# Optimization experiments

Hardware: AMD Instinct MI355X
Metric: run time of the kernel (lower is better)

Reference implementation:

```python
import jax, jax.numpy as jnp
import numpy as np

N = 50000   # nodes
E = 800000  # edges (avg degree 16)
D = 128     # feature dim
H = 4       # heads
DH = D // H # head dim


def setup_inputs() -> dict:
    key = jax.random.key(0)
    ks = jax.random.split(key, 12)
    s = 1.0 / np.sqrt(D)
    return {
        "x": jax.random.normal(ks[0], (N, D), dtype=jnp.float32),
        "src": jax.random.randint(ks[1], (E,), 0, N, dtype=jnp.int32),
        "dst": jax.random.randint(ks[2], (E,), 0, N, dtype=jnp.int32),
        # input_linear: Linear(d, d)
        "W_in": jax.random.uniform(ks[3], (D, D), jnp.float32, -s, s),
        "b_in": jax.random.uniform(ks[4], (D,), jnp.float32, -s, s),
        # attn_linear_u: Linear(d, n_heads), attn_linear_v: Linear(d, n_heads, bias=False)
        "W_au": jax.random.uniform(ks[5], (D, H), jnp.float32, -s, s),
        "b_au": jax.random.uniform(ks[6], (H,), jnp.float32, -s, s),
        "W_av": jax.random.uniform(ks[7], (D, H), jnp.float32, -s, s),
        # FFN: Linear(d, d) -> ReLU -> Linear(d, d)  (dropout=0)
        "W_f1": jax.random.uniform(ks[8], (D, D), jnp.float32, -s, s),
        "b_f1": jax.random.uniform(ks[9], (D,), jnp.float32, -s, s),
        "W_f2": jax.random.uniform(ks[10], (D, D), jnp.float32, -s, s),
        "b_f2": jax.random.uniform(ks[11], (D,), jnp.float32, -s, s),
    }


def reference(x, src, dst, W_in, b_in, W_au, b_au, W_av, W_f1, b_f1, W_f2, b_f2):
    h = x @ W_in + b_in                                # [N, D]
    su = h @ W_au + b_au                               # [N, H]
    sv = h @ W_av                                      # [N, H]
    # u_add_v gather + LeakyReLU
    e = jax.nn.leaky_relu(su[src] + sv[dst], 0.2)      # [E, H]
    # edge_softmax: softmax over incoming edges of each dst node
    m = jax.ops.segment_max(e, dst, num_segments=N)    # [N, H]
    ex = jnp.exp(e - m[dst])                           # [E, H]
    z = jax.ops.segment_sum(ex, dst, num_segments=N)   # [N, H]
    p = ex / z[dst]                                    # [E, H]
    # u_mul_e_sum: weighted aggregation (note reshape order (N, d_head, H))
    hu = h.reshape(N, DH, H)[src]                      # [E, DH, H]
    agg = jax.ops.segment_sum(hu * p[:, None, :], dst, num_segments=N)  # [N, DH, H]
    y = agg.reshape(N, D)
    # FFN
    return jax.nn.relu(y @ W_f1 + b_f1) @ W_f2 + b_f2
```

## Files before the change

### kernel.cpp

```cpp
#include <hip/hip_runtime.h>
#include <hip/hip_bf16.h>
#include <math.h>

#define D 128
#define NHEADS 4

static constexpr int CAP  = 64;
static constexpr int CAPB = 5120;
static constexpr int EB   = 4096;

typedef __attribute__((ext_vector_type(8))) short bf16x8;
typedef __attribute__((ext_vector_type(4))) float f32x4;

__device__ __forceinline__ float4 ld4(const float* p) {
    return *reinterpret_cast<const float4*>(p);
}
__device__ __forceinline__ float4 fma4(float a, float4 b, float4 c) {
    c.x = fmaf(a, b.x, c.x); c.y = fmaf(a, b.y, c.y);
    c.z = fmaf(a, b.z, c.z); c.w = fmaf(a, b.w, c.w);
    return c;
}
__device__ __forceinline__ unsigned short f2bf(float f) {
    __hip_bfloat16 b = __float2bfloat16(f);
    return __builtin_bit_cast(unsigned short, b);
}
__device__ __forceinline__ float bf2f(unsigned short u) {
    return __uint_as_float((unsigned)u << 16);
}
__device__ __forceinline__ void cvt_hilo(const float4& a0, const float4& a1,
                                         bf16x8& hi, bf16x8& lo) {
    float v[8] = {a0.x, a0.y, a0.z, a0.w, a1.x, a1.y, a1.z, a1.w};
#pragma unroll
    for (int i = 0; i < 8; ++i) {
        unsigned short h = f2bf(v[i]);
        hi[i] = (short)h;
        lo[i] = (short)f2bf(v[i] - bf2f(h));
    }
}

__global__ __launch_bounds__(256)
void clear_kernel(int* __restrict__ bucket_cnt, int nb16) {
    for (int i = threadIdx.x; i < nb16; i += 256) bucket_cnt[i] = 0;
}

template<int MODE>
__global__ __launch_bounds__(256)
void mfma_gemm128(const float* __restrict__ A, const float* __restrict__ W,
                  const float* __restrict__ bias, float* __restrict__ out,
                  unsigned short* __restrict__ out16, int N, int ntiles)
{
    __shared__ unsigned short wh[D * D];
    __shared__ unsigned short wl[D * D];

    const int t = threadIdx.x;
#pragma unroll
    for (int i = 0; i < 16; ++i) {
        int g = t + i * 256;
        int col = g & 127;
        int k0 = (g >> 7) << 2;
        short4 h4, l4;
#pragma unroll
        for (int k = 0; k < 4; ++k) {
            float v = W[(size_t)(k0 + k) * D + col];
            unsigned short hb = f2bf(v);
            ((short*)&h4)[k] = (short)hb;
            ((short*)&l4)[k] = (short)f2bf(v - bf2f(hb));
        }
        int off = col * D + (k0 ^ ((col & 7) << 3));
        *reinterpret_cast<short4*>(&wh[off]) = h4;
        *reinterpret_cast<short4*>(&wl[off]) = l4;
    }
    __syncthreads();

    const int wid  = t >> 6;
    const int lane = t & 63;
    const int q8   = (lane >> 4) * 8;

    for (int tile = blockIdx.x; tile < ntiles; tile += gridDim.x) {
        const int rbase = tile * 64 + wid * 16;
        const int arow  = rbase + (lane & 15);

        bf16x8 ahi[4], alo[4];
#pragma unroll
        for (int ks = 0; ks < 4; ++ks) {
            float4 a0 = {0, 0, 0, 0}, a1 = {0, 0, 0, 0};
            if (arow < N) {
                const float* ap = A + (size_t)arow * D + 32 * ks + q8;
                a0 = ld4(ap); a1 = ld4(ap + 4);
            }
            cvt_hilo(a0, a1, ahi[ks], alo[ks]);
        }

        f32x4 acc[8];
#pragma unroll
        for (int ct = 0; ct < 8; ++ct) acc[ct] = (f32x4){0.f, 0.f, 0.f, 0.f};

#pragma unroll
        for (int ct = 0; ct < 8; ++ct) {
            const int colb = ct * 16 + (lane & 15);
            const int sw   = (colb & 7) << 3;
            bf16x8 bh[4], bl[4];
#pragma unroll
            for (int ks = 0; ks < 4; ++ks) {
                int off = colb * D + ((32 * ks + q8) ^ sw);
                bh[ks] = *reinterpret_cast<const bf16x8*>(&wh[off]);
                bl[ks] = *reinterpret_cast<const bf16x8*>(&wl[off]);
            }
#pragma unroll
            for (int ks = 0; ks < 4; ++ks) {
                acc[ct] = __builtin_amdgcn_mfma_f32_16x16x32_bf16(ahi[ks], bh[ks], acc[ct], 0, 0, 0);
                acc[ct] = __builtin_amdgcn_mfma_f32_16x16x32_bf16(alo[ks], bh[ks], acc[ct], 0, 0, 0);
                acc[ct] = __builtin_amdgcn_mfma_f32_16x16x32_bf16(ahi[ks], bl[ks], acc[ct], 0, 0, 0);
            }
        }

        const int crow0 = rbase + (lane >> 4) * 4;
#pragma unroll
        for (int ct = 0; ct < 8; ++ct) {
            const int col = ct * 16 + (lane & 15);
            const float bv = bias[col];
#pragma unroll
            for (int j = 0; j < 4; ++j) {
                const int r = crow0 + j;
                if (r < N) {
                    float v = acc[ct][j] + bv;
                    if constexpr (MODE == 1) v = fmaxf(v, 0.f);
                    if constexpr (MODE == 0)
                        out16[(size_t)r * D + col] = f2bf(v);
                    else
                        out[(size_t)r * D + col] = v;
                }
            }
        }
    }
}

__global__ __launch_bounds__(256)
void att_scores_kernel(const unsigned short* __restrict__ h16,
                       const float* __restrict__ Wau, const float* __restrict__ bau,
                       const float* __restrict__ Wav,
                       float* __restrict__ su, float* __restrict__ sv, int N)
{
    const int wid  = threadIdx.x >> 6;
    const int lane = threadIdx.x & 63;
    const int n = blockIdx.x * 4 + wid;
    if (n >= N) return;

    const int c = lane * 2;
    unsigned u = *reinterpret_cast<const unsigned*>(h16 + (size_t)n * D + c);
    const float hx = __uint_as_float(u << 16);
    const float hy = __uint_as_float(u & 0xffff0000u);

    float4 s_u = {0, 0, 0, 0}, s_v = {0, 0, 0, 0};
    s_u = fma4(hx, ld4(Wau + c * NHEADS), s_u);
    s_u = fma4(hy, ld4(Wau + (c + 1) * NHEADS), s_u);
    s_v = fma4(hx, ld4(Wav + c * NHEADS), s_v);
    s_v = fma4(hy, ld4(Wav + (c + 1) * NHEADS), s_v);

#pragma unroll
    for (int d2 = 1; d2 < 64; d2 <<= 1) {
        s_u.x += __shfl_xor(s_u.x, d2); s_u.y += __shfl_xor(s_u.y, d2);
        s_u.z += __shfl_xor(s_u.z, d2); s_u.w += __shfl_xor(s_u.w, d2);
        s_v.x += __shfl_xor(s_v.x, d2); s_v.y += __shfl_xor(s_v.y, d2);
        s_v.z += __shfl_xor(s_v.z, d2); s_v.w += __shfl_xor(s_v.w, d2);
    }
    if (lane == 0) {
        float4 ub = ld4(bau);
        s_u.x += ub.x; s_u.y += ub.y; s_u.z += ub.z; s_u.w += ub.w;
        *reinterpret_cast<float4*>(su + (size_t)n * NHEADS) = s_u;
        *reinterpret_cast<float4*>(sv + (size_t)n * NHEADS) = s_v;
    }
}

__global__ __launch_bounds__(256)
void bin_kernel(const int* __restrict__ src, const int* __restrict__ dst,
                int* __restrict__ bucket_cnt ,
                unsigned* __restrict__ bucket_buf, int E, int NB)
{
    __shared__ int hist[256];
    __shared__ int base[256];
    __shared__ int off[256];
    const int t = threadIdx.x;
    hist[t] = 0; off[t] = 0;
    __syncthreads();

    const int e0 = blockIdx.x * EB;
#pragma unroll
    for (int j = 0; j < EB / 256; ++j) {
        int idx = e0 + j * 256 + t;
        if (idx < E) atomicAdd(&hist[dst[idx] >> 8], 1);
    }
    __syncthreads();
    if (t < NB) {
        int hv = hist[t];
        base[t] = hv ? atomicAdd(&bucket_cnt[t * 16], hv) : 0;
    }
    __syncthreads();
#pragma unroll
    for (int j = 0; j < EB / 256; ++j) {
        int idx = e0 + j * 256 + t;
        if (idx < E) {
            int d = dst[idx];
            int b = d >> 8;
            int p = base[b] + atomicAdd(&off[b], 1);
            if (p < CAPB)
                bucket_buf[(size_t)b * CAPB + p] =
                    (unsigned)(src[idx] | ((d & 255) << 16));
        }
    }
}

__global__ __launch_bounds__(256)
void csr_kernel(const int* __restrict__ bucket_cnt, const unsigned* __restrict__ bucket_buf,
                unsigned short* __restrict__ slot, int* __restrict__ deg, int N)
{
    __shared__ unsigned ebuf[CAPB];
    __shared__ int cur[256];
    const int b = blockIdx.x;
    const int t = threadIdx.x;
    const int cnt = min(bucket_cnt[b * 16], CAPB);
    cur[t] = 0;
    for (int i = t; i < cnt; i += 256)
        ebuf[i] = bucket_buf[(size_t)b * CAPB + i];
    __syncthreads();
    for (int i = t; i < cnt; i += 256) {
        unsigned e = ebuf[i];
        int dl = e >> 16;
        int pos = atomicAdd(&cur[dl], 1);
        if (pos < CAP)
            slot[(((size_t)(b * 256 + dl)) << 6) + pos] = (unsigned short)(e & 0xffff);
    }
    __syncthreads();
    int n = b * 256 + t;
    if (n < N) deg[n] = min(cur[t], CAP);
}

__global__ __launch_bounds__(256)
void agg_kernel(const unsigned short* __restrict__ h16, const float* __restrict__ su,
                const float* __restrict__ sv, const int* __restrict__ deg_arr,
                const unsigned short* __restrict__ slot, float* __restrict__ y, int N)
{
    __shared__ int   s_s[4][64];
    __shared__ float s_p[4][64][4];

    const int wslot = threadIdx.x >> 6;
    const int lane  = threadIdx.x & 63;
    const int n = blockIdx.x * 4 + wslot;
    if (n >= N) return;

    const int deg = deg_arr[n];

    if (deg == 0) {
        *reinterpret_cast<float2*>(y + (size_t)n * D + lane * 2) = float2{0.f, 0.f};
        return;
    }

    const float4 sv4 = ld4(sv + (size_t)n * NHEADS);

    float4 z4 = {0.f, 0.f, 0.f, 0.f};
    float2 acc = {0.f, 0.f};
    const int psel = (lane & 1) * 2;

    int sj = 0;
    float4 ex4 = {0.f, 0.f, 0.f, 0.f};
    if (lane < deg) {
        sj = slot[((size_t)n << 6) + lane];
        float4 u = ld4(su + (size_t)sj * NHEADS);
        float e0 = u.x + sv4.x, e1 = u.y + sv4.y, e2 = u.z + sv4.z, e3 = u.w + sv4.w;
        e0 = e0 >= 0.f ? e0 : 0.2f * e0; e1 = e1 >= 0.f ? e1 : 0.2f * e1;
        e2 = e2 >= 0.f ? e2 : 0.2f * e2; e3 = e3 >= 0.f ? e3 : 0.2f * e3;
        ex4.x = __expf(e0); ex4.y = __expf(e1);
        ex4.z = __expf(e2); ex4.w = __expf(e3);
    }
    float4 tt = ex4;
#pragma unroll
    for (int d2 = 1; d2 < 64; d2 <<= 1) {
        tt.x += __shfl_xor(tt.x, d2); tt.y += __shfl_xor(tt.y, d2);
        tt.z += __shfl_xor(tt.z, d2); tt.w += __shfl_xor(tt.w, d2);
    }
    z4.x += tt.x; z4.y += tt.y; z4.z += tt.z; z4.w += tt.w;

    s_s[wslot][lane] = sj;
    *reinterpret_cast<float4*>(&s_p[wslot][lane][0]) = ex4;
    __builtin_amdgcn_wave_barrier();

#pragma unroll 4
    for (int j = 0; j < deg; ++j) {
        int s = s_s[wslot][j];
        float2 p2 = *reinterpret_cast<const float2*>(&s_p[wslot][j][psel]);
        unsigned u = *reinterpret_cast<const unsigned*>(h16 + ((size_t)s << 7) + (lane << 1));
        acc.x = fmaf(p2.x, __uint_as_float(u << 16), acc.x);
        acc.y = fmaf(p2.y, __uint_as_float(u & 0xffff0000u), acc.y);
    }

    const float2 z2 = (lane & 1) ? float2{z4.z, z4.w} : float2{z4.x, z4.y};
    float2 o;
    o.x = acc.x / z2.x;
    o.y = acc.y / z2.y;
    *reinterpret_cast<float2*>(y + (size_t)n * D + lane * 2) = o;
}

extern "C" void kernel_launch(void* const* d_in, const int* in_sizes, int n_in,
                              void* d_out, int out_size, void* d_ws, size_t ws_size,
                              hipStream_t stream) {
    const float* x    = (const float*)d_in[0];
    const int*   src  = (const int*)d_in[1];
    const int*   dst  = (const int*)d_in[2];
    const float* W_in = (const float*)d_in[3];
    const float* b_in = (const float*)d_in[4];
    const float* W_au = (const float*)d_in[5];
    const float* b_au = (const float*)d_in[6];
    const float* W_av = (const float*)d_in[7];
    const float* W_f1 = (const float*)d_in[8];
    const float* b_f1 = (const float*)d_in[9];
    const float* W_f2 = (const float*)d_in[10];
    const float* b_f2 = (const float*)d_in[11];
    float* out = (float*)d_out;

    const int N = in_sizes[0] / D;
    const int E = in_sizes[1];
    const int NB = (N + 255) / 256;

    char* ws = (char*)d_ws;
    size_t o = 0;
    auto alloc = [&](size_t bytes) -> void* {
        void* p = ws + o;
        o += (bytes + 255) & ~(size_t)255;
        return p;
    };
    void*           bufA       = alloc((size_t)N * D * 4);
    float*          y          = (float*)alloc((size_t)N * D * 4);
    float*          su         = (float*)alloc((size_t)N * NHEADS * 4);
    float*          sv         = (float*)alloc((size_t)N * NHEADS * 4);
    int*            bucket_cnt = (int*)alloc((size_t)NB * 16 * 4);
    unsigned*       bucket_buf = (unsigned*)alloc((size_t)NB * CAPB * 4);
    unsigned short* slot       = (unsigned short*)alloc((size_t)NB * 256 * CAP * 2);
    int*            deg        = (int*)alloc((size_t)N * 4);

    unsigned short* h16 = (unsigned short*)bufA;
    float*          hid = (float*)bufA;

    const int bgrid  = (E + EB - 1) / EB;
    const int ntiles = (N + 63) / 64;
    const int ggrid  = (ntiles + 1) / 2;

    clear_kernel<<<1, 256, 0, stream>>>(bucket_cnt, NB * 16);

    bin_kernel<<<bgrid, 256, 0, stream>>>(src, dst, bucket_cnt, bucket_buf, E, NB);

    mfma_gemm128<0><<<ggrid, 256, 0, stream>>>(x, W_in, b_in, nullptr, h16, N, ntiles);

    csr_kernel<<<NB, 256, 0, stream>>>(bucket_cnt, bucket_buf, slot, deg, N);

    att_scores_kernel<<<(N + 3) / 4, 256, 0, stream>>>(h16, W_au, b_au, W_av, su, sv, N);

    agg_kernel<<<(N + 3) / 4, 256, 0, stream>>>(h16, su, sv, deg, slot, y, N);

    mfma_gemm128<1><<<ggrid, 256, 0, stream>>>(y, W_f1, b_f1, hid, nullptr, N, ntiles);
    mfma_gemm128<2><<<ggrid, 256, 0, stream>>>(hid, W_f2, b_f2, out, nullptr, N, ntiles);
}
```

Measured before the change: 153.0 us.

## Fuse CSR build with attention scores and batch gather loads in aggregation

Merges the CSR slot-building kernel and the attention score kernel into one launch, with block ranges split by index so the two independent workloads run concurrently. The aggregation loop now issues up to eight neighbor row loads before consuming them, to increase memory-level parallelism. The binning block size is halved for more blocks. The fused kernel reserves the large shared buffer for all blocks, which may reduce occupancy of the attention part.

```diff
diff --git a/kernel.cpp b/kernel.cpp
--- a/kernel.cpp
+++ b/kernel.cpp
@@ -7,7 +7,7 @@
 
 static constexpr int CAP  = 64;
 static constexpr int CAPB = 5120;
-static constexpr int EB   = 4096;
+static constexpr int EB   = 2048;
 
 typedef __attribute__((ext_vector_type(8))) short bf16x8;
 typedef __attribute__((ext_vector_type(4))) float f32x4;
@@ -136,43 +136,6 @@
 }
 
 __global__ __launch_bounds__(256)
-void att_scores_kernel(const unsigned short* __restrict__ h16,
-                       const float* __restrict__ Wau, const float* __restrict__ bau,
-                       const float* __restrict__ Wav,
-                       float* __restrict__ su, float* __restrict__ sv, int N)
-{
-    const int wid  = threadIdx.x >> 6;
-    const int lane = threadIdx.x & 63;
-    const int n = blockIdx.x * 4 + wid;
-    if (n >= N) return;
-
-    const int c = lane * 2;
-    unsigned u = *reinterpret_cast<const unsigned*>(h16 + (size_t)n * D + c);
-    const float hx = __uint_as_float(u << 16);
-    const float hy = __uint_as_float(u & 0xffff0000u);
-
-    float4 s_u = {0, 0, 0, 0}, s_v = {0, 0, 0, 0};
-    s_u = fma4(hx, ld4(Wau + c * NHEADS), s_u);
-    s_u = fma4(hy, ld4(Wau + (c + 1) * NHEADS), s_u);
-    s_v = fma4(hx, ld4(Wav + c * NHEADS), s_v);
-    s_v = fma4(hy, ld4(Wav + (c + 1) * NHEADS), s_v);
-
-#pragma unroll
-    for (int d2 = 1; d2 < 64; d2 <<= 1) {
-        s_u.x += __shfl_xor(s_u.x, d2); s_u.y += __shfl_xor(s_u.y, d2);
-        s_u.z += __shfl_xor(s_u.z, d2); s_u.w += __shfl_xor(s_u.w, d2);
-        s_v.x += __shfl_xor(s_v.x, d2); s_v.y += __shfl_xor(s_v.y, d2);
-        s_v.z += __shfl_xor(s_v.z, d2); s_v.w += __shfl_xor(s_v.w, d2);
-    }
-    if (lane == 0) {
-        float4 ub = ld4(bau);
-        s_u.x += ub.x; s_u.y += ub.y; s_u.z += ub.z; s_u.w += ub.w;
-        *reinterpret_cast<float4*>(su + (size_t)n * NHEADS) = s_u;
-        *reinterpret_cast<float4*>(sv + (size_t)n * NHEADS) = s_v;
-    }
-}
-
-__global__ __launch_bounds__(256)
 void bin_kernel(const int* __restrict__ src, const int* __restrict__ dst,
                 int* __restrict__ bucket_cnt ,
                 unsigned* __restrict__ bucket_buf, int E, int NB)
@@ -211,28 +174,66 @@
 }
 
 __global__ __launch_bounds__(256)
-void csr_kernel(const int* __restrict__ bucket_cnt, const unsigned* __restrict__ bucket_buf,
-                unsigned short* __restrict__ slot, int* __restrict__ deg, int N)
+void csr_att_kernel(const int* __restrict__ bucket_cnt, const unsigned* __restrict__ bucket_buf,
+                    unsigned short* __restrict__ slot, int* __restrict__ deg, int N, int NB,
+                    const unsigned short* __restrict__ h16,
+                    const float* __restrict__ Wau, const float* __restrict__ bau,
+                    const float* __restrict__ Wav,
+                    float* __restrict__ su, float* __restrict__ sv)
 {
     __shared__ unsigned ebuf[CAPB];
     __shared__ int cur[256];
-    const int b = blockIdx.x;
+
     const int t = threadIdx.x;
-    const int cnt = min(bucket_cnt[b * 16], CAPB);
-    cur[t] = 0;
-    for (int i = t; i < cnt; i += 256)
-        ebuf[i] = bucket_buf[(size_t)b * CAPB + i];
-    __syncthreads();
-    for (int i = t; i < cnt; i += 256) {
-        unsigned e = ebuf[i];
-        int dl = e >> 16;
-        int pos = atomicAdd(&cur[dl], 1);
-        if (pos < CAP)
-            slot[(((size_t)(b * 256 + dl)) << 6) + pos] = (unsigned short)(e & 0xffff);
-    }
-    __syncthreads();
-    int n = b * 256 + t;
-    if (n < N) deg[n] = min(cur[t], CAP);
+    if ((int)blockIdx.x < NB) {
+        const int b = blockIdx.x;
+        const int cnt = min(bucket_cnt[b * 16], CAPB);
+        cur[t] = 0;
+        for (int i = t; i < cnt; i += 256)
+            ebuf[i] = bucket_buf[(size_t)b * CAPB + i];
+        __syncthreads();
+        for (int i = t; i < cnt; i += 256) {
+            unsigned e = ebuf[i];
+            int dl = e >> 16;
+            int pos = atomicAdd(&cur[dl], 1);
+            if (pos < CAP)
+                slot[(((size_t)(b * 256 + dl)) << 6) + pos] = (unsigned short)(e & 0xffff);
+        }
+        __syncthreads();
+        int n = b * 256 + t;
+        if (n < N) deg[n] = min(cur[t], CAP);
+        return;
+    }
+
+    const int wid  = t >> 6;
+    const int lane = t & 63;
+    const int n = (blockIdx.x - NB) * 4 + wid;
+    if (n >= N) return;
+
+    const int c = lane * 2;
+    unsigned u = *reinterpret_cast<const unsigned*>(h16 + (size_t)n * D + c);
+    const float hx = __uint_as_float(u << 16);
+    const float hy = __uint_as_float(u & 0xffff0000u);
+
+    float4 s_u = {0, 0, 0, 0}, s_v = {0, 0, 0, 0};
+    s_u = fma4(hx, ld4(Wau + c * NHEADS), s_u);
+    s_u = fma4(hy, ld4(Wau + (c + 1) * NHEADS), s_u);
+    s_v = fma4(hx, ld4(Wav + c * NHEADS), s_v);
+    s_v = fma4(hy, ld4(Wav + (c + 1) * NHEADS), s_v);
+
+#pragma unroll
+    for (int d2 = 1; d2 < 64; d2 <<= 1) {
+        s_u.x += __shfl_xor(s_u.x, d2); s_u.y += __shfl_xor(s_u.y, d2);
+        s_u.z += __shfl_xor(s_u.z, d2); s_u.w += __shfl_xor(s_u.w, d2);
+        s_v.x += __shfl_xor(s_v.x, d2); s_v.y += __shfl_xor(s_v.y, d2);
+        s_v.z += __shfl_xor(s_v.z, d2); s_v.w += __shfl_xor(s_v.w, d2);
+    }
+    if (lane == 0) {
+        float4 ub = ld4(bau);
+        s_u.x += ub.x; s_u.y += ub.y; s_u.z += ub.z; s_u.w += ub.w;
+        *reinterpret_cast<float4*>(su + (size_t)n * NHEADS) = s_u;
+        *reinterpret_cast<float4*>(sv + (size_t)n * NHEADS) = s_v;
+    }
 }
 
 __global__ __launch_bounds__(256)
@@ -257,8 +258,6 @@
 
     const float4 sv4 = ld4(sv + (size_t)n * NHEADS);
 
-    float4 z4 = {0.f, 0.f, 0.f, 0.f};
-    float2 acc = {0.f, 0.f};
     const int psel = (lane & 1) * 2;
 
     int sj = 0;
@@ -272,25 +271,37 @@
         ex4.x = __expf(e0); ex4.y = __expf(e1);
         ex4.z = __expf(e2); ex4.w = __expf(e3);
     }
-    float4 tt = ex4;
+    float4 z4 = ex4;
 #pragma unroll
     for (int d2 = 1; d2 < 64; d2 <<= 1) {
-        tt.x += __shfl_xor(tt.x, d2); tt.y += __shfl_xor(tt.y, d2);
-        tt.z += __shfl_xor(tt.z, d2); tt.w += __shfl_xor(tt.w, d2);
-    }
-    z4.x += tt.x; z4.y += tt.y; z4.z += tt.z; z4.w += tt.w;
+        z4.x += __shfl_xor(z4.x, d2); z4.y += __shfl_xor(z4.y, d2);
+        z4.z += __shfl_xor(z4.z, d2); z4.w += __shfl_xor(z4.w, d2);
+    }
 
     s_s[wslot][lane] = sj;
     *reinterpret_cast<float4*>(&s_p[wslot][lane][0]) = ex4;
     __builtin_amdgcn_wave_barrier();
 
-#pragma unroll 4
-    for (int j = 0; j < deg; ++j) {
-        int s = s_s[wslot][j];
-        float2 p2 = *reinterpret_cast<const float2*>(&s_p[wslot][j][psel]);
-        unsigned u = *reinterpret_cast<const unsigned*>(h16 + ((size_t)s << 7) + (lane << 1));
-        acc.x = fmaf(p2.x, __uint_as_float(u << 16), acc.x);
-        acc.y = fmaf(p2.y, __uint_as_float(u & 0xffff0000u), acc.y);
+    float2 acc = {0.f, 0.f};
+    for (int j0 = 0; j0 < deg; j0 += 8) {
+        const int je = (deg - j0 < 8) ? (deg - j0) : 8;
+        unsigned hv[8];
+        float2   pv[8];
+#pragma unroll
+        for (int k = 0; k < 8; ++k) {
+            if (k < je) {
+                int s = s_s[wslot][j0 + k];
+                hv[k] = *reinterpret_cast<const unsigned*>(h16 + ((size_t)s << 7) + (lane << 1));
+                pv[k] = *reinterpret_cast<const float2*>(&s_p[wslot][j0 + k][psel]);
+            }
+        }
+#pragma unroll
+        for (int k = 0; k < 8; ++k) {
+            if (k < je) {
+                acc.x = fmaf(pv[k].x, __uint_as_float(hv[k] << 16), acc.x);
+                acc.y = fmaf(pv[k].y, __uint_as_float(hv[k] & 0xffff0000u), acc.y);
+            }
+        }
     }
 
     const float2 z2 = (lane & 1) ? float2{z4.z, z4.w} : float2{z4.x, z4.y};
@@ -343,6 +354,7 @@
     const int bgrid  = (E + EB - 1) / EB;
     const int ntiles = (N + 63) / 64;
     const int ggrid  = (ntiles + 1) / 2;
+    const int agrid  = (N + 3) / 4;
 
     clear_kernel<<<1, 256, 0, stream>>>(bucket_cnt, NB * 16);
 
@@ -350,11 +362,10 @@
 
     mfma_gemm128<0><<<ggrid, 256, 0, stream>>>(x, W_in, b_in, nullptr, h16, N, ntiles);
 
-    csr_kernel<<<NB, 256, 0, stream>>>(bucket_cnt, bucket_buf, slot, deg, N);
-
-    att_scores_kernel<<<(N + 3) / 4, 256, 0, stream>>>(h16, W_au, b_au, W_av, su, sv, N);
-
-    agg_kernel<<<(N + 3) / 4, 256, 0, stream>>>(h16, su, sv, deg, slot, y, N);
+    csr_att_kernel<<<NB + agrid, 256, 0, stream>>>(bucket_cnt, bucket_buf, slot, deg, N, NB,
+                                                   h16, W_au, b_au, W_av, su, sv);
+
+    agg_kernel<<<agrid, 256, 0, stream>>>(h16, su, sv, deg, slot, y, N);
 
     mfma_gemm128<1><<<ggrid, 256, 0, stream>>>(y, W_f1, b_f1, hid, nullptr, N, ntiles);
     mfma_gemm128<2><<<ggrid, 256, 0, stream>>>(hid, W_f2, b_f2, out, nullptr, N, ntiles);
```

Result: faster. 146.0 us (-4.6%).
